# Performance work log

Hardware: AMD Instinct MI355X
Metric: run time of the kernel (lower is better)

The kernel has to match this reference:

```python
import jax, jax.numpy as jnp
import numpy as np

B, N, C, H, KC, STAGES = 8, 4096, 256, 8, 128, 3
C4 = 4 * C
HD = C4 // H
SCALE = (C // H) ** -0.5  # torch uses head_dim of ORIGINAL dim: (256//8)^-0.5


def _l2norm(x, axis):
    # torch: inp / (1e-6 + inp.norm(dim=axis, keepdim=True))
    return x / (1e-6 + jnp.linalg.norm(x, axis=axis, keepdims=True))


def _dta_branch(xc):
    """EM-style clustering on one stream. xc: [B, 4C, N] -> bases [B, 4C, KC]."""
    b, c, n = xc.shape
    # AdaptiveMaxPool1d(KC): N % KC == 0 -> uniform windows of size N//KC
    bases = _l2norm(xc.reshape(b, c, KC, n // KC).max(axis=-1), axis=1)
    xn = xc.transpose(0, 2, 1)  # [B, N, 4C]
    for _ in range(STAGES):
        z = jax.nn.softmax(jnp.einsum('bnc,bck->bnk', xn, bases), axis=2)  # [B,N,KC]
        z = _l2norm(z, axis=1)
        bases = _l2norm(jnp.einsum('bnc,bnk->bck', xn, z), axis=1)  # [B,4C,KC]
    return bases


def setup_inputs() -> dict:
    key = jax.random.key(0)
    ks = jax.random.split(key, 6)
    x = jax.random.normal(ks[0], (B, N, C), jnp.float32)
    Wq = jax.random.normal(ks[1], (C4, C), jnp.float32) * 0.02
    Wk = jax.random.normal(ks[2], (C4, C), jnp.float32) * 0.02
    Wv = jax.random.normal(ks[3], (C4, C), jnp.float32) * 0.02
    Wp = jax.random.normal(ks[4], (C, C4), jnp.float32) * 0.02
    bp = jnp.zeros((C,), jnp.float32)
    return {"x": x, "Wq": Wq, "Wk": Wk, "Wv": Wv, "Wp": Wp, "bp": bp}


def reference(x, Wq, Wk, Wv, Wp, bp):
    # q/k/v projections (bias-free), [B,N,4C]
    q = x @ Wq.T
    k = x @ Wk.T
    v = x @ Wv.T
    # DTA: note torch does `q, k = self.DA(q, k)` where DA(x1,x2) returns
    # (bases_from_x1, bases_from_x2) -> q bases from q-stream, k bases from k-stream.
    qb = _dta_branch(q.transpose(0, 2, 1))  # [B,4C,KC]
    kb = _dta_branch(k.transpose(0, 2, 1))  # [B,4C,KC]
    qh = qb.reshape(B, H, HD, KC)  # == torch q.permute(0,1,3,2): [B,H,hd,KC]
    kh = kb.reshape(B, H, HD, KC)
    vh = v.transpose(0, 2, 1).reshape(B, H, HD, N)  # [B,H,hd,N]
    # att over cluster axis KC -> [B,H,hd,hd]
    att = jax.nn.softmax(jnp.einsum('bhdk,bhek->bhde', qh, kh) * SCALE, axis=-1)
    o = jnp.einsum('bhde,bhen->bhdn', att, vh)  # [B,H,hd,N]
    # rearrange 'b n_h head_dim n -> b n (n_h head_dim)'
    o = o.transpose(0, 3, 1, 2).reshape(B, N, C4)
    return jax.nn.relu(o @ Wp.T + bp)
```

## Files before the change

kernel.cpp:

```cpp
#include <hip/hip_runtime.h>
#include <hip/hip_bf16.h>

#define NSEQ 4096
#define C4   1024
#define SCALE_F 0.17677669529663687f
#define SLC   524288

typedef __attribute__((ext_vector_type(8))) short bf16x8;
typedef __attribute__((ext_vector_type(4))) float f32x4;
typedef __attribute__((ext_vector_type(8))) unsigned short u16x8;
typedef __attribute__((ext_vector_type(4))) unsigned short u16x4;

__device__ __forceinline__ unsigned short f2b(float x){
  union{float f; unsigned u;} v; v.f = x;
  unsigned r = v.u + 0x7fffu + ((v.u>>16)&1u);
  return (unsigned short)(r>>16);
}
__device__ __forceinline__ unsigned mapf(float x){
  unsigned u = __float_as_uint(x);
  return (u & 0x80000000u) ? ~u : (u | 0x80000000u);
}
__device__ __forceinline__ float unmapf(unsigned m){
  unsigned u = (m & 0x80000000u) ? (m ^ 0x80000000u) : ~m;
  return __uint_as_float(u);
}

typedef __attribute__((address_space(1))) void* gas_p;
typedef __attribute__((address_space(3))) void* las_p;
#define GLDS16(gp, lp) __builtin_amdgcn_global_load_lds((gas_p)(gp), (las_p)(lp), 16, 0, 0)

#define WAITVM8() asm volatile("s_waitcnt vmcnt(8)" ::: "memory")
#define WAITVM4() asm volatile("s_waitcnt vmcnt(4)" ::: "memory")
#define WAITVM0() asm volatile("s_waitcnt vmcnt(0)" ::: "memory")
#define WAITLGKM() asm volatile("s_waitcnt lgkmcnt(0)" ::: "memory")
__device__ __forceinline__ void barrier(){
  asm volatile("" ::: "memory");
  __builtin_amdgcn_s_barrier();
  asm volatile("" ::: "memory");
}

__device__ __forceinline__ void stage128x64s(const unsigned short* G, int row0, int ld, int k0,
                                             unsigned short* lds, int tid){
#pragma unroll
  for (int i = 0; i < 4; ++i){
    int cid = i*256 + tid;
    int r = cid >> 3, c8 = cid & 7;
    GLDS16(G + (row0 + r)*ld + k0 + ((c8 ^ (r & 7))*8), lds + cid*8);
  }
}

__device__ __forceinline__ void stage128x128s(const unsigned short* G, int row0, int ld, int k0,
                                              unsigned short* lds, int tid){
#pragma unroll
  for (int i = 0; i < 8; ++i){
    int cid = i*256 + tid;
    int r = cid >> 4, c16 = cid & 15;
    GLDS16(G + (row0 + r)*ld + k0 + ((c16 ^ (r & 7))*8), lds + cid*8);
  }
}

template<int LD, int NK, int MA, int MB>
__device__ __forceinline__ void mma_tiles(const unsigned short* ldsA, const unsigned short* ldsB,
                                          f32x4 acc[4][4], int wr, int wc, int lane){
  const int rowg = lane & 15, q4 = lane >> 4;
#pragma unroll
  for (int kc = 0; kc < NK; ++kc){
    bf16x8 a[4], b[4];
#pragma unroll
    for (int mf = 0; mf < 4; ++mf){
      int row = wr*64 + mf*16 + rowg;
      int off;
      if constexpr (MA == 1) off = ((kc*4 + q4) ^ (row & 7)) * 8;
      else                   off = kc*32 + q4*8;
      a[mf] = *(const bf16x8*)(ldsA + row*LD + off);
    }
#pragma unroll
    for (int nf = 0; nf < 4; ++nf){
      int col = wc*64 + nf*16 + rowg;
      int off;
      if constexpr (MB == 1)      off = ((kc*4 + q4) ^ (col & 7)) * 8;
      else if constexpr (MB == 2) off = (kc*32 + q4*8) ^ ((((col>>3) ^ col) & 7) << 3);
      else                        off = kc*32 + q4*8;
      b[nf] = *(const bf16x8*)(ldsB + col*LD + off);
    }
#pragma unroll
    for (int mf = 0; mf < 4; ++mf)
#pragma unroll
      for (int nf = 0; nf < 4; ++nf)
        acc[mf][nf] = __builtin_amdgcn_mfma_f32_16x16x32_bf16(a[mf], b[nf], acc[mf][nf], 0, 0, 0);
  }
}

__global__ __launch_bounds__(256) void k_cast(const float* __restrict__ src,
                                              unsigned short* __restrict__ dst,
                                              unsigned* __restrict__ pooled, int n){
  int i = (blockIdx.x*256 + threadIdx.x) * 4;
  if (i < n){
    float4 v = *(const float4*)(src + i);
    u16x4 o = { f2b(v.x), f2b(v.y), f2b(v.z), f2b(v.w) };
    *(u16x4*)(dst + i) = o;
  }
  if (blockIdx.x < 2048){
    uint4 z = {0u, 0u, 0u, 0u};
    *(uint4*)(pooled + (blockIdx.x*256 + threadIdx.x)*4) = z;
  }
}

__global__ __launch_bounds__(256) void k_wprep(const float* __restrict__ Wq, const float* __restrict__ Wk,
                                               const float* __restrict__ Wv, const float* __restrict__ Wp,
                                               unsigned short* __restrict__ Wcat,
                                               unsigned short* __restrict__ Wpbf,
                                               unsigned short* __restrict__ WcatT,
                                               unsigned short* __restrict__ WvT){
  int t = blockIdx.x*256 + threadIdx.x;
  int s = blockIdx.y;
  if (s < 3){
    const float* src = (s == 0) ? Wq : (s == 1) ? Wk : Wp;
    unsigned short* dst = (s == 0) ? Wcat : (s == 1) ? (Wcat + 262144) : Wpbf;
    int i = t*4;
    float4 v = *(const float4*)(src + i);
    u16x4 o = { f2b(v.x), f2b(v.y), f2b(v.z), f2b(v.w) };
    *(u16x4*)(dst + i) = o;
  } else {
    const float* src = (s == 3) ? Wv : (s == 4) ? Wq : Wk;
    unsigned short* dst = (s == 3) ? WvT : WcatT;
    int ld  = (s == 3) ? 1024 : 2048;
    int off = (s == 5) ? 1024 : 0;
    int j = t & 255, r0 = (t >> 8) * 4;
    u16x4 o = { f2b(src[(r0+0)*256 + j]), f2b(src[(r0+1)*256 + j]),
                f2b(src[(r0+2)*256 + j]), f2b(src[(r0+3)*256 + j]) };
    *(u16x4*)(dst + j*ld + off + r0) = o;
  }
}

__global__ __launch_bounds__(256) void k_gemm_qk(const unsigned short* __restrict__ xbf,
                                                 const unsigned short* __restrict__ Wcat,
                                                 unsigned* __restrict__ pooled){
  __shared__ __align__(16) unsigned short ldsA[128*64];
  __shared__ __align__(16) unsigned short ldsB[128*64];
  int tid = threadIdx.x, lane = tid & 63, wid = tid >> 6, wr = wid >> 1, wc = wid & 1;
  int m0 = blockIdx.x*128, n0 = blockIdx.y*128;
  f32x4 acc[4][4] = {};
  for (int k0 = 0; k0 < 256; k0 += 64){
    __syncthreads();
    stage128x64s(xbf,  m0, 256, k0, ldsA, tid);
    stage128x64s(Wcat, n0, 256, k0, ldsB, tid);
    __syncthreads();
    mma_tiles<64,2,1,1>(ldsA, ldsB, acc, wr, wc, lane);
  }
  int colg = lane & 15;
  int b = m0 >> 12, kbase = (m0 & 4095) >> 5;
#pragma unroll
  for (int nf = 0; nf < 4; ++nf){
    float wlo = -3e38f, whi = -3e38f;
#pragma unroll
    for (int r = 0; r < 4; ++r){
      wlo = fmaxf(wlo, fmaxf(acc[0][nf][r], acc[1][nf][r]));
      whi = fmaxf(whi, fmaxf(acc[2][nf][r], acc[3][nf][r]));
    }
    wlo = fmaxf(wlo, __shfl_xor(wlo, 16)); wlo = fmaxf(wlo, __shfl_xor(wlo, 32));
    whi = fmaxf(whi, __shfl_xor(whi, 16)); whi = fmaxf(whi, __shfl_xor(whi, 32));
    if (lane < 16){
      int col = n0 + wc*64 + nf*16 + colg;
      int sbp = b + ((col >> 10) << 3);
      int c4 = col & 1023;
      atomicMax(&pooled[(sbp*128 + kbase + wr*2    )*C4 + c4], mapf(wlo));
      atomicMax(&pooled[(sbp*128 + kbase + wr*2 + 1)*C4 + c4], mapf(whi));
    }
  }
}

__global__ __launch_bounds__(256) void k_norm(const float* __restrict__ bRaw,
                                              const unsigned* __restrict__ pooled,
                                              unsigned short* __restrict__ basesT, int S){
  int row = blockIdx.x, tid = threadIdx.x, lane = tid & 63, wid = tid >> 6;
  float4 v;
  if (S == 0){
    uint4 u = *(const uint4*)(pooled + row*C4 + tid*4);
    v.x = unmapf(u.x); v.y = unmapf(u.y); v.z = unmapf(u.z); v.w = unmapf(u.w);
  } else {
    v = *(const float4*)(bRaw + row*C4 + tid*4);
  }
  float ss = v.x*v.x + v.y*v.y + v.z*v.z + v.w*v.w;
  __shared__ float red[5];
#pragma unroll
  for (int o = 32; o; o >>= 1) ss += __shfl_down(ss, o);
  if (lane == 0) red[wid] = ss;
  __syncthreads();
  if (tid == 0) red[4] = 1.f / (1e-6f + sqrtf(red[0] + red[1] + red[2] + red[3]));
  __syncthreads();
  float inv = red[4];
  u16x4 o4 = { f2b(v.x*inv), f2b(v.y*inv), f2b(v.z*inv), f2b(v.w*inv) };
  *(u16x4*)(basesT + row*C4 + tid*4) = o4;
}

__global__ __launch_bounds__(256) void k_pb(const unsigned short* __restrict__ basesT,
                                            const unsigned short* __restrict__ WcatT,
                                            float* __restrict__ part){
  __shared__ __align__(16) unsigned short ldsA[128*64];
  __shared__ __align__(16) unsigned short ldsB[128*64];
  int tid = threadIdx.x, lane = tid & 63, wid = tid >> 6, wr = wid >> 1, wc = wid & 1;
  int n0 = blockIdx.x*128, sb = blockIdx.y, ks = blockIdx.z;
  const unsigned short* A = basesT + sb*(128*C4);
  int off = (sb >= 8) ? 1024 : 0;
  f32x4 acc[4][4] = {};
  for (int t = 0; t < 4; ++t){
    __syncthreads();
    stage128x64s(A,     0,  C4,   ks*256 + t*64, ldsA, tid);
    stage128x64s(WcatT, n0, 2048, off + ks*256 + t*64, ldsB, tid);
    __syncthreads();
    mma_tiles<64,2,1,1>(ldsA, ldsB, acc, wr, wc, lane);
  }
  int colg = lane & 15, rowg = (lane >> 4) * 4;
#pragma unroll
  for (int mf = 0; mf < 4; ++mf)
#pragma unroll
    for (int nf = 0; nf < 4; ++nf)
#pragma unroll
      for (int r = 0; r < 4; ++r)
        part[ks*SLC + (sb*128 + wr*64 + mf*16 + rowg + r)*256 + n0 + wc*64 + nf*16 + colg]
          = acc[mf][nf][r];
}

__global__ __launch_bounds__(256) void k_redgt(const float* __restrict__ src,
                                               unsigned short* __restrict__ dst, int S){
  int i = (blockIdx.x*256 + threadIdx.x) * 4;
  float4 a = {0.f,0.f,0.f,0.f};
  for (int s = 0; s < S; ++s){
    float4 u = *(const float4*)(src + s*SLC + i);
    a.x += u.x; a.y += u.y; a.z += u.z; a.w += u.w;
  }
  u16x4 o = { f2b(a.x), f2b(a.y), f2b(a.z), f2b(a.w) };
  *(u16x4*)(dst + i) = o;
}

__global__ __launch_bounds__(256) void k_gemm_z(const unsigned short* __restrict__ xbf,
                                                const unsigned short* __restrict__ PBT,
                                                unsigned short* __restrict__ zT){
  __shared__ __align__(16) unsigned short smem[32768];
  __shared__ float redb[2][2][128];
  unsigned short* zt = smem;
  int tid = threadIdx.x, lane = tid & 63, wid = tid >> 6, wr = wid >> 1, wc = wid & 1;
  int m0 = blockIdx.x*128, sb = blockIdx.y;
  const unsigned short* A = xbf + (sb & 7)*(NSEQ*256);
  const unsigned short* B = PBT + sb*(128*256);
  f32x4 acc[4][4] = {};
  stage128x64s(A, m0, 256, 0, smem, tid);
  stage128x64s(B, 0,  256, 0, smem + 16384, tid);
  for (int t = 0; t < 4; ++t){
    int cur = t & 1;
    if (t < 3){
      stage128x64s(A, m0, 256, (t+1)*64, smem + (cur^1)*8192, tid);
      stage128x64s(B, 0,  256, (t+1)*64, smem + 16384 + (cur^1)*8192, tid);
      WAITVM8();
    } else WAITVM0();
    barrier();
    mma_tiles<64,2,1,1>(smem + cur*8192, smem + 16384 + cur*8192, acc, wr, wc, lane);
    WAITLGKM();
    barrier();
  }
  int colg = lane & 15, rowg = (lane >> 4) * 4;
  float sm[4][4];
#pragma unroll
  for (int mf = 0; mf < 4; ++mf)
#pragma unroll
    for (int r = 0; r < 4; ++r){
      float m = fmaxf(fmaxf(acc[mf][0][r], acc[mf][1][r]), fmaxf(acc[mf][2][r], acc[mf][3][r]));
#pragma unroll
      for (int o = 1; o < 16; o <<= 1) m = fmaxf(m, __shfl_xor(m, o));
      if (colg == 0) redb[0][wc][wr*64 + mf*16 + rowg + r] = m;
    }
  barrier();
#pragma unroll
  for (int mf = 0; mf < 4; ++mf)
#pragma unroll
    for (int r = 0; r < 4; ++r){
      int idx = wr*64 + mf*16 + rowg + r;
      float m = fmaxf(redb[0][0][idx], redb[0][1][idx]);
      float s = 0.f;
#pragma unroll
      for (int nf = 0; nf < 4; ++nf){
        float e = __expf(acc[mf][nf][r] - m);
        acc[mf][nf][r] = e; s += e;
      }
#pragma unroll
      for (int o = 1; o < 16; o <<= 1) s += __shfl_xor(s, o);
      if (colg == 0) redb[1][wc][idx] = s;
    }
  barrier();
#pragma unroll
  for (int mf = 0; mf < 4; ++mf)
#pragma unroll
    for (int r = 0; r < 4; ++r){
      int idx = wr*64 + mf*16 + rowg + r;
      sm[mf][r] = 1.f / (redb[1][0][idx] + redb[1][1][idx]);
    }
#pragma unroll
  for (int mf = 0; mf < 4; ++mf)
#pragma unroll
    for (int nf = 0; nf < 4; ++nf){
      int k = wc*64 + nf*16 + colg;
      int swz = (k & 7) << 3;
#pragma unroll
      for (int r = 0; r < 4; ++r){
        int n = wr*64 + mf*16 + rowg + r;
        zt[k*128 + (n ^ swz)] = f2b(acc[mf][nf][r] * sm[mf][r]);
      }
    }
  WAITLGKM();
  barrier();
#pragma unroll
  for (int i = 0; i < 8; ++i){
    int cid = i*256 + tid;
    int kk = cid >> 4, j8 = cid & 15;
    int nbase = (j8*8) ^ ((kk & 7) << 3);
    *(uint4*)(zT + sb*(128*NSEQ) + kk*NSEQ + m0 + nbase) = *(const uint4*)(zt + kk*128 + j8*8);
  }
}

__global__ __launch_bounds__(256) void k_gemm_gt(const unsigned short* __restrict__ xbf,
                                                 const unsigned short* __restrict__ zT,
                                                 float* __restrict__ part){
  __shared__ __align__(16) unsigned short ldsA[2][8192];
  __shared__ __align__(16) unsigned short ldsB[2][8192];
  int tid = threadIdx.x, lane = tid & 63, wid = tid >> 6, wr = wid >> 1, wc = wid & 1;
  int c0 = blockIdx.x*128, sb = blockIdx.y, ks = blockIdx.z;
  const unsigned short* xb = xbf + (sb & 7)*(NSEQ*256);
  const unsigned short* Zt = zT + sb*(128*NSEQ);
  int base = ks*512;
  f32x4 acc[4][4] = {};
  u16x8 vB[4];
  int np_[4], c8_[4];
#pragma unroll
  for (int i = 0; i < 4; ++i){
    int cid = i*256 + tid;
    np_[i] = cid >> 4; c8_[i] = cid & 15;
  }
  stage128x64s(Zt, 0, NSEQ, base, ldsA[0], tid);
#pragma unroll
  for (int i = 0; i < 4; ++i)
    vB[i] = *(const u16x8*)(xb + (base + np_[i])*256 + c0 + c8_[i]*8);
  for (int t = 0; t < 8; ++t){
    int cur = t & 1, n0 = base + t*64;
    if (t < 7){
      stage128x64s(Zt, 0, NSEQ, n0 + 64, ldsA[cur^1], tid);
      WAITVM4();
    } else WAITVM0();
#pragma unroll
    for (int i = 0; i < 4; ++i){
#pragma unroll
      for (int j = 0; j < 8; ++j)
        ldsB[cur][(c8_[i]*8 + j)*64 + (np_[i] ^ (((c8_[i] ^ j) & 7) << 3))] = vB[i][j];
    }
    WAITLGKM();
    barrier();
    if (t < 7){
#pragma unroll
      for (int i = 0; i < 4; ++i)
        vB[i] = *(const u16x8*)(xb + (n0 + 64 + np_[i])*256 + c0 + c8_[i]*8);
    }
    mma_tiles<64,2,1,2>(ldsA[cur], ldsB[cur], acc, wr, wc, lane);
    WAITLGKM();
    barrier();
  }
  int colg = lane & 15, rowg = (lane >> 4) * 4;
#pragma unroll
  for (int mf = 0; mf < 4; ++mf)
#pragma unroll
    for (int nf = 0; nf < 4; ++nf)
#pragma unroll
      for (int r = 0; r < 4; ++r)
        part[ks*SLC + (sb*128 + wr*64 + mf*16 + rowg + r)*256 + c0 + wc*64 + nf*16 + colg]
          = acc[mf][nf][r];
}

__global__ __launch_bounds__(256) void k_pbases(const unsigned short* __restrict__ Wcat,
                                                const unsigned short* __restrict__ GTbf,
                                                float* __restrict__ bRaw){
  __shared__ __align__(16) unsigned short ldsA[128*64];
  __shared__ __align__(16) unsigned short ldsB[128*64];
  int tid = threadIdx.x, lane = tid & 63, wid = tid >> 6, wr = wid >> 1, wc = wid & 1;
  int m0 = blockIdx.x*128, sb = blockIdx.y;
  const unsigned short* A = Wcat + ((sb >= 8) ? 1024*256 : 0);
  const unsigned short* B = GTbf + sb*(128*256);
  f32x4 acc[4][4] = {};
  for (int t = 0; t < 4; ++t){
    __syncthreads();
    stage128x64s(A, m0, 256, t*64, ldsA, tid);
    stage128x64s(B, 0,  256, t*64, ldsB, tid);
    __syncthreads();
    mma_tiles<64,2,1,1>(ldsA, ldsB, acc, wr, wc, lane);
  }
  int colg = lane & 15, rowg = (lane >> 4) * 4;
#pragma unroll
  for (int mf = 0; mf < 4; ++mf)
#pragma unroll
    for (int nf = 0; nf < 4; ++nf)
#pragma unroll
      for (int r = 0; r < 4; ++r){
        int c4 = m0 + wr*64 + mf*16 + rowg + r;
        int k  = wc*64 + nf*16 + colg;
        bRaw[(sb*128 + k)*C4 + c4] = acc[mf][nf][r];
      }
}

__global__ __launch_bounds__(256) void k_attnwp(const unsigned short* __restrict__ basesT,
                                                const unsigned short* __restrict__ Wpbf,
                                                unsigned short* __restrict__ WpEff){
  __shared__ __align__(16) char smem[98816];
  unsigned short* Qlt = (unsigned short*)smem;
  unsigned short* Klt = (unsigned short*)(smem + 32768);
  float* scores       = (float*)smem;
  unsigned short* at  = (unsigned short*)(smem + 66048);
  unsigned short* Wl  = (unsigned short*)smem;
  int tid = threadIdx.x, lane = tid & 63, wid = tid >> 6, wr = wid >> 1, wc = wid & 1;
  int m0 = blockIdx.x*128;
  int bh = blockIdx.y, b = bh >> 3, h = bh & 7;
  const unsigned short* Q = basesT + b*(128*C4) + h*128;
  const unsigned short* K = basesT + (8 + b)*(128*C4) + h*128;
#pragma unroll
  for (int i = 0; i < 8; ++i){
    int cid = i*256 + tid, kk = cid >> 4, c8 = cid & 15;
    u16x8 vq = *(const u16x8*)(Q + kk*C4 + c8*8);
    u16x8 vk = *(const u16x8*)(K + kk*C4 + c8*8);
#pragma unroll
    for (int j = 0; j < 8; ++j){
      Qlt[(c8*8 + j)*128 + kk] = vq[j];
      Klt[(c8*8 + j)*128 + kk] = vk[j];
    }
  }
  __syncthreads();
  f32x4 acc[4][4] = {};
  mma_tiles<128,4,0,0>(Qlt, Klt, acc, wr, wc, lane);
  __syncthreads();
  int colg = lane & 15, rowg = (lane >> 4) * 4;
#pragma unroll
  for (int mf = 0; mf < 4; ++mf)
#pragma unroll
    for (int nf = 0; nf < 4; ++nf)
#pragma unroll
      for (int r = 0; r < 4; ++r)
        scores[(wr*64 + mf*16 + rowg + r)*129 + wc*64 + nf*16 + colg] = acc[mf][nf][r] * SCALE_F;
  __syncthreads();
  if (tid < 128){
    float mx = -3e38f;
    for (int j = 0; j < 128; ++j) mx = fmaxf(mx, scores[tid*129 + j]);
    float s = 0.f;
    for (int j = 0; j < 128; ++j){ float e = __expf(scores[tid*129 + j] - mx); scores[tid*129 + j] = e; s += e; }
    float inv = 1.f / s;
    for (int j = 0; j < 128; ++j) at[j*128 + tid] = f2b(scores[tid*129 + j] * inv);
  }
  __syncthreads();
  stage128x128s(Wpbf, m0, C4, h*128, Wl, tid);
  __syncthreads();
  f32x4 acc2[4][4] = {};
  mma_tiles<128,4,1,0>(Wl, at, acc2, wr, wc, lane);
#pragma unroll
  for (int mf = 0; mf < 4; ++mf)
#pragma unroll
    for (int nf = 0; nf < 4; ++nf)
#pragma unroll
      for (int r = 0; r < 4; ++r){
        int row = m0 + wr*64 + mf*16 + rowg + r;
        int col = wc*64 + nf*16 + colg;
        WpEff[b*(256*C4) + row*C4 + h*128 + col] = f2b(acc2[mf][nf][r]);
      }
}

__global__ __launch_bounds__(256) void k_gemm_w2(const unsigned short* __restrict__ WpEff,
                                                 const unsigned short* __restrict__ WvT,
                                                 unsigned short* __restrict__ W2){
  __shared__ __align__(16) unsigned short ldsA[128*64];
  __shared__ __align__(16) unsigned short ldsB[128*64];
  int tid = threadIdx.x, lane = tid & 63, wid = tid >> 6, wr = wid >> 1, wc = wid & 1;
  int m0 = blockIdx.x*128, n0 = blockIdx.y*128, b = blockIdx.z;
  const unsigned short* A = WpEff + b*(256*C4);
  f32x4 acc[4][4] = {};
  for (int k0 = 0; k0 < C4; k0 += 64){
    __syncthreads();
    stage128x64s(A,   m0, C4, k0, ldsA, tid);
    stage128x64s(WvT, n0, C4, k0, ldsB, tid);
    __syncthreads();
    mma_tiles<64,2,1,1>(ldsA, ldsB, acc, wr, wc, lane);
  }
  int colg = lane & 15, rowg = (lane >> 4) * 4;
#pragma unroll
  for (int mf = 0; mf < 4; ++mf)
#pragma unroll
    for (int nf = 0; nf < 4; ++nf)
#pragma unroll
      for (int r = 0; r < 4; ++r){
        int row = m0 + wr*64 + mf*16 + rowg + r;
        int col = n0 + wc*64 + nf*16 + colg;
        W2[b*65536 + row*256 + col] = f2b(acc[mf][nf][r]);
      }
}

__global__ __launch_bounds__(256) void k_gemm_out(const unsigned short* __restrict__ xbf,
                                                  const unsigned short* __restrict__ W2,
                                                  const float* __restrict__ bp,
                                                  float* __restrict__ out){
  __shared__ __align__(16) unsigned short ldsA[2][8192];
  __shared__ __align__(16) unsigned short ldsB[2][8192];
  int tid = threadIdx.x, lane = tid & 63, wid = tid >> 6, wr = wid >> 1, wc = wid & 1;
  int m0 = blockIdx.x*128, n0 = blockIdx.y*128, b = blockIdx.z;
  const unsigned short* A = xbf + b*(NSEQ*256);
  const unsigned short* Bm = W2 + b*65536;
  f32x4 acc[4][4] = {};
  stage128x64s(A,  m0, 256, 0, ldsA[0], tid);
  stage128x64s(Bm, n0, 256, 0, ldsB[0], tid);
  for (int t = 0; t < 4; ++t){
    int cur = t & 1;
    if (t < 3){
      stage128x64s(A,  m0, 256, (t+1)*64, ldsA[cur^1], tid);
      stage128x64s(Bm, n0, 256, (t+1)*64, ldsB[cur^1], tid);
      WAITVM8();
    } else WAITVM0();
    barrier();
    mma_tiles<64,2,1,1>(ldsA[cur], ldsB[cur], acc, wr, wc, lane);
    WAITLGKM();
    barrier();
  }
  int colg = lane & 15, rowg = (lane >> 4) * 4;
#pragma unroll
  for (int mf = 0; mf < 4; ++mf)
#pragma unroll
    for (int nf = 0; nf < 4; ++nf){
      int col = n0 + wc*64 + nf*16 + colg;
      float bias = bp[col];
#pragma unroll
      for (int r = 0; r < 4; ++r){
        int row = m0 + wr*64 + mf*16 + rowg + r;
        out[(b*NSEQ + row)*256 + col] = fmaxf(acc[mf][nf][r] + bias, 0.f);
      }
    }
}

extern "C" void kernel_launch(void* const* d_in, const int* in_sizes, int n_in,
                              void* d_out, int out_size, void* d_ws, size_t ws_size,
                              hipStream_t stream){
  (void)in_sizes; (void)n_in; (void)out_size; (void)ws_size;
  const float* x  = (const float*)d_in[0];
  const float* Wq = (const float*)d_in[1];
  const float* Wk = (const float*)d_in[2];
  const float* Wv = (const float*)d_in[3];
  const float* Wp = (const float*)d_in[4];
  const float* bp = (const float*)d_in[5];
  float* out = (float*)d_out;
  char* ws = (char*)d_ws;

  unsigned short* xbf    = (unsigned short*)(ws + 0);
  unsigned short* zT     = (unsigned short*)(ws + 16777216);
  float*          bPart  = (float*)(ws + 33554432);
  unsigned*       pooled = (unsigned*)(ws + 50331648);
  float*          bRawP  = (float*)(ws + 58720256);
  unsigned short* basesT = (unsigned short*)(ws + 67108864);
  unsigned short* WpEff  = (unsigned short*)(ws + 71303168);
  unsigned short* PBT    = (unsigned short*)(ws + 77594624);
  unsigned short* GTbf   = (unsigned short*)(ws + 78643200);
  unsigned short* Wcat   = (unsigned short*)(ws + 79691776);
  unsigned short* WcatT  = (unsigned short*)(ws + 80740352);
  unsigned short* W2     = (unsigned short*)(ws + 81788928);
  unsigned short* WvT    = (unsigned short*)(ws + 82837504);
  unsigned short* Wpbf   = (unsigned short*)(ws + 83361792);

  k_cast<<<8192, 256, 0, stream>>>(x, xbf, pooled, 8388608);
  k_wprep<<<dim3(256, 6), 256, 0, stream>>>(Wq, Wk, Wv, Wp, Wcat, Wpbf, WcatT, WvT);

  k_gemm_qk<<<dim3(256, 16), 256, 0, stream>>>(xbf, Wcat, pooled);
  k_norm<<<2048, 256, 0, stream>>>(bRawP, pooled, basesT, 0);

  for (int st = 0; st < 3; ++st){
    k_pb<<<dim3(2, 16, 4), 256, 0, stream>>>(basesT, WcatT, bPart);
    k_redgt<<<512, 256, 0, stream>>>(bPart, PBT, 4);
    k_gemm_z<<<dim3(32, 16), 256, 0, stream>>>(xbf, PBT, zT);
    k_gemm_gt<<<dim3(2, 16, 8), 256, 0, stream>>>(xbf, zT, bPart);
    k_redgt<<<512, 256, 0, stream>>>(bPart, GTbf, 8);
    k_pbases<<<dim3(8, 16), 256, 0, stream>>>(Wcat, GTbf, bRawP);
    k_norm<<<2048, 256, 0, stream>>>(bRawP, pooled, basesT, 1);
  }

  k_attnwp<<<dim3(2, 64), 256, 0, stream>>>(basesT, Wpbf, WpEff);
  k_gemm_w2<<<dim3(2, 2, 8), 256, 0, stream>>>(WpEff, WvT, W2);
  k_gemm_out<<<dim3(32, 2, 8), 256, 0, stream>>>(xbf, W2, bp, out);
}
```

Measured before the change: 288.9 us.

## Fuse split-K reductions into GEMM kernels via last-block atomic counter

Removes the separate k_redgt reduction launches by having the last split-K block for each output tile (detected with an atomic counter plus thread fences) sum the partials and write the bf16 result. Counters are reset inside k_norm, which runs before each use. This saves six kernel launches per forward pass and their launch gaps. In exchange the reduction now runs serially in one block per tile, and correctness depends on fence ordering and on the counter reset.

```diff
diff --git a/kernel.cpp b/kernel.cpp
--- a/kernel.cpp
+++ b/kernel.cpp
@@ -172,7 +172,9 @@
 
 __global__ __launch_bounds__(256) void k_norm(const float* __restrict__ bRaw,
                                               const unsigned* __restrict__ pooled,
-                                              unsigned short* __restrict__ basesT, int S){
+                                              unsigned short* __restrict__ basesT,
+                                              unsigned* __restrict__ cnt, int S){
+  if (blockIdx.x == 0 && threadIdx.x < 64) cnt[threadIdx.x] = 0u;
   int row = blockIdx.x, tid = threadIdx.x, lane = tid & 63, wid = tid >> 6;
   float4 v;
   if (S == 0){
@@ -196,9 +198,12 @@
 
 __global__ __launch_bounds__(256) void k_pb(const unsigned short* __restrict__ basesT,
                                             const unsigned short* __restrict__ WcatT,
-                                            float* __restrict__ part){
+                                            float* __restrict__ part,
+                                            unsigned short* __restrict__ PBT,
+                                            unsigned* __restrict__ cnt){
   __shared__ __align__(16) unsigned short ldsA[128*64];
   __shared__ __align__(16) unsigned short ldsB[128*64];
+  __shared__ unsigned lastFlag;
   int tid = threadIdx.x, lane = tid & 63, wid = tid >> 6, wr = wid >> 1, wc = wid & 1;
   int n0 = blockIdx.x*128, sb = blockIdx.y, ks = blockIdx.z;
   const unsigned short* A = basesT + sb*(128*C4);
@@ -220,18 +225,31 @@
       for (int r = 0; r < 4; ++r)
         part[ks*SLC + (sb*128 + wr*64 + mf*16 + rowg + r)*256 + n0 + wc*64 + nf*16 + colg]
           = acc[mf][nf][r];
-}
-
-__global__ __launch_bounds__(256) void k_redgt(const float* __restrict__ src,
-                                               unsigned short* __restrict__ dst, int S){
-  int i = (blockIdx.x*256 + threadIdx.x) * 4;
-  float4 a = {0.f,0.f,0.f,0.f};
-  for (int s = 0; s < S; ++s){
-    float4 u = *(const float4*)(src + s*SLC + i);
-    a.x += u.x; a.y += u.y; a.z += u.z; a.w += u.w;
-  }
-  u16x4 o = { f2b(a.x), f2b(a.y), f2b(a.z), f2b(a.w) };
-  *(u16x4*)(dst + i) = o;
+  WAITVM0();
+  __syncthreads();
+  if (tid == 0){
+    __threadfence();
+    unsigned old = atomicAdd(&cnt[blockIdx.x*16 + sb], 1u);
+    lastFlag = (old == 3u) ? 1u : 0u;
+  }
+  __syncthreads();
+  if (lastFlag){
+    __threadfence();
+    const float* base = part + (sb*128)*256 + n0;
+#pragma unroll
+    for (int i = 0; i < 16; ++i){
+      int e = i*256 + tid;
+      int row = e >> 5, c4 = (e & 31)*4;
+      float4 a = {0.f,0.f,0.f,0.f};
+#pragma unroll
+      for (int s = 0; s < 4; ++s){
+        float4 u = *(const float4*)(base + s*SLC + row*256 + c4);
+        a.x += u.x; a.y += u.y; a.z += u.z; a.w += u.w;
+      }
+      u16x4 o = { f2b(a.x), f2b(a.y), f2b(a.z), f2b(a.w) };
+      *(u16x4*)(PBT + (sb*128 + row)*256 + n0 + c4) = o;
+    }
+  }
 }
 
 __global__ __launch_bounds__(256) void k_gemm_z(const unsigned short* __restrict__ xbf,
@@ -320,9 +338,12 @@
 
 __global__ __launch_bounds__(256) void k_gemm_gt(const unsigned short* __restrict__ xbf,
                                                  const unsigned short* __restrict__ zT,
-                                                 float* __restrict__ part){
+                                                 float* __restrict__ part,
+                                                 unsigned short* __restrict__ GTbf,
+                                                 unsigned* __restrict__ cnt){
   __shared__ __align__(16) unsigned short ldsA[2][8192];
   __shared__ __align__(16) unsigned short ldsB[2][8192];
+  __shared__ unsigned lastFlag;
   int tid = threadIdx.x, lane = tid & 63, wid = tid >> 6, wr = wid >> 1, wc = wid & 1;
   int c0 = blockIdx.x*128, sb = blockIdx.y, ks = blockIdx.z;
   const unsigned short* xb = xbf + (sb & 7)*(NSEQ*256);
@@ -372,6 +393,31 @@
       for (int r = 0; r < 4; ++r)
         part[ks*SLC + (sb*128 + wr*64 + mf*16 + rowg + r)*256 + c0 + wc*64 + nf*16 + colg]
           = acc[mf][nf][r];
+  WAITVM0();
+  __syncthreads();
+  if (tid == 0){
+    __threadfence();
+    unsigned old = atomicAdd(&cnt[32 + blockIdx.x*16 + sb], 1u);
+    lastFlag = (old == 7u) ? 1u : 0u;
+  }
+  __syncthreads();
+  if (lastFlag){
+    __threadfence();
+    const float* basep = part + (sb*128)*256 + c0;
+#pragma unroll
+    for (int i = 0; i < 16; ++i){
+      int e = i*256 + tid;
+      int row = e >> 5, c4 = (e & 31)*4;
+      float4 a = {0.f,0.f,0.f,0.f};
+#pragma unroll
+      for (int s = 0; s < 8; ++s){
+        float4 u = *(const float4*)(basep + s*SLC + row*256 + c4);
+        a.x += u.x; a.y += u.y; a.z += u.z; a.w += u.w;
+      }
+      u16x4 o = { f2b(a.x), f2b(a.y), f2b(a.z), f2b(a.w) };
+      *(u16x4*)(GTbf + (sb*128 + row)*256 + c0 + c4) = o;
+    }
+  }
 }
 
 __global__ __launch_bounds__(256) void k_pbases(const unsigned short* __restrict__ Wcat,
@@ -563,21 +609,20 @@
   unsigned short* W2     = (unsigned short*)(ws + 81788928);
   unsigned short* WvT    = (unsigned short*)(ws + 82837504);
   unsigned short* Wpbf   = (unsigned short*)(ws + 83361792);
+  unsigned*       cnt    = (unsigned*)(ws + 83886080);
 
   k_cast<<<8192, 256, 0, stream>>>(x, xbf, pooled, 8388608);
   k_wprep<<<dim3(256, 6), 256, 0, stream>>>(Wq, Wk, Wv, Wp, Wcat, Wpbf, WcatT, WvT);
 
   k_gemm_qk<<<dim3(256, 16), 256, 0, stream>>>(xbf, Wcat, pooled);
-  k_norm<<<2048, 256, 0, stream>>>(bRawP, pooled, basesT, 0);
+  k_norm<<<2048, 256, 0, stream>>>(bRawP, pooled, basesT, cnt, 0);
 
   for (int st = 0; st < 3; ++st){
-    k_pb<<<dim3(2, 16, 4), 256, 0, stream>>>(basesT, WcatT, bPart);
-    k_redgt<<<512, 256, 0, stream>>>(bPart, PBT, 4);
+    k_pb<<<dim3(2, 16, 4), 256, 0, stream>>>(basesT, WcatT, bPart, PBT, cnt);
     k_gemm_z<<<dim3(32, 16), 256, 0, stream>>>(xbf, PBT, zT);
-    k_gemm_gt<<<dim3(2, 16, 8), 256, 0, stream>>>(xbf, zT, bPart);
-    k_redgt<<<512, 256, 0, stream>>>(bPart, GTbf, 8);
+    k_gemm_gt<<<dim3(2, 16, 8), 256, 0, stream>>>(xbf, zT, bPart, GTbf, cnt);
     k_pbases<<<dim3(8, 16), 256, 0, stream>>>(Wcat, GTbf, bRawP);
-    k_norm<<<2048, 256, 0, stream>>>(bRawP, pooled, basesT, 1);
+    k_norm<<<2048, 256, 0, stream>>>(bRawP, pooled, basesT, cnt, 1);
   }
 
   k_attnwp<<<dim3(2, 64), 256, 0, stream>>>(basesT, Wpbf, WpEff);
```

Measured after the change: 345.2 us. 1.2x slower.

## Fold bases projection through precomputed weight Gram matrix in EM iterations

Applied to the files above, without the earlier changes.

Precomputes the 256x256 Gram matrix of the Q and K weights once, then in EM stages 2 and 3 computes the normalized projected bases directly from the reduced G^T via a small fused GEMM with the Gram matrix. The norm uses the quadratic form g^T Gram g. This replaces the per-stage k_pbases, k_norm, k_pb and reduction launches with one 16-block kernel. It adds a bf16 Gram matrix and a norm computed from it, which may change rounding, and the fused kernel runs on only 16 blocks.

```diff
diff --git a/kernel.cpp b/kernel.cpp
--- a/kernel.cpp
+++ b/kernel.cpp
@@ -11,6 +11,9 @@
 typedef __attribute__((ext_vector_type(8))) unsigned short u16x8;
 typedef __attribute__((ext_vector_type(4))) unsigned short u16x4;
 
+__device__ __forceinline__ float b2f(unsigned short b){
+  union{unsigned u; float f;} v; v.u = ((unsigned)b)<<16; return v.f;
+}
 __device__ __forceinline__ unsigned short f2b(float x){
   union{float f; unsigned u;} v; v.f = x;
   unsigned r = v.u + 0x7fffu + ((v.u>>16)&1u);
@@ -57,6 +60,11 @@
     int r = cid >> 4, c16 = cid & 15;
     GLDS16(G + (row0 + r)*ld + k0 + ((c16 ^ (r & 7))*8), lds + cid*8);
   }
+}
+
+__device__ __forceinline__ float gtread(const unsigned short* gtile, int row, int c){
+  int p = c >> 6, cc = c & 63, c8g = cc >> 3, j = cc & 7;
+  return b2f(gtile[p*8192 + row*64 + ((c8g ^ (row & 7)) << 3) + j]);
 }
 
 template<int LD, int NK, int MA, int MB>
@@ -133,6 +141,31 @@
   }
 }
 
+__global__ __launch_bounds__(256) void k_gram(const unsigned short* __restrict__ WcatT,
+                                              unsigned short* __restrict__ Gram){
+  __shared__ __align__(16) unsigned short ldsA[128*64];
+  __shared__ __align__(16) unsigned short ldsB[128*64];
+  int tid = threadIdx.x, lane = tid & 63, wid = tid >> 6, wr = wid >> 1, wc = wid & 1;
+  int m0 = blockIdx.x*128, n0 = blockIdx.y*128, off = blockIdx.z*1024;
+  f32x4 acc[4][4] = {};
+  for (int k0 = 0; k0 < 1024; k0 += 64){
+    __syncthreads();
+    stage128x64s(WcatT, m0, 2048, off + k0, ldsA, tid);
+    stage128x64s(WcatT, n0, 2048, off + k0, ldsB, tid);
+    __syncthreads();
+    mma_tiles<64,2,1,1>(ldsA, ldsB, acc, wr, wc, lane);
+  }
+  int colg = lane & 15, rowg = (lane >> 4) * 4;
+#pragma unroll
+  for (int mf = 0; mf < 4; ++mf)
+#pragma unroll
+    for (int nf = 0; nf < 4; ++nf)
+#pragma unroll
+      for (int r = 0; r < 4; ++r)
+        Gram[blockIdx.z*65536 + (m0 + wr*64 + mf*16 + rowg + r)*256 + n0 + wc*64 + nf*16 + colg]
+          = f2b(acc[mf][nf][r]);
+}
+
 __global__ __launch_bounds__(256) void k_gemm_qk(const unsigned short* __restrict__ xbf,
                                                  const unsigned short* __restrict__ Wcat,
                                                  unsigned* __restrict__ pooled){
@@ -232,6 +265,66 @@
   }
   u16x4 o = { f2b(a.x), f2b(a.y), f2b(a.z), f2b(a.w) };
   *(u16x4*)(dst + i) = o;
+}
+
+__global__ __launch_bounds__(256) void k_normpb(const unsigned short* __restrict__ GTbf,
+                                                const unsigned short* __restrict__ Gram,
+                                                unsigned short* __restrict__ PBT){
+  __shared__ __align__(16) unsigned short gtile[128*256];
+  __shared__ __align__(16) unsigned short btile[128*64];
+  __shared__ float redn[2][128];
+  int tid = threadIdx.x, lane = tid & 63, wid = tid >> 6, wr = wid >> 1, wc = wid & 1;
+  int sb = blockIdx.x;
+  const unsigned short* GTsb = GTbf + sb*(128*256);
+  const unsigned short* Gm = Gram + ((sb >= 8) ? 65536 : 0);
+#pragma unroll
+  for (int p = 0; p < 4; ++p)
+    stage128x64s(GTsb, 0, 256, p*64, gtile + p*8192, tid);
+  f32x4 accA[4][4] = {}, accB[4][4] = {};
+  for (int t = 0; t < 4; ++t){
+    __syncthreads();
+    stage128x64s(Gm, 0, 256, t*64, btile, tid);
+    __syncthreads();
+    mma_tiles<64,2,1,1>(gtile + t*8192, btile, accA, wr, wc, lane);
+  }
+  for (int t = 0; t < 4; ++t){
+    __syncthreads();
+    stage128x64s(Gm, 128, 256, t*64, btile, tid);
+    __syncthreads();
+    mma_tiles<64,2,1,1>(gtile + t*8192, btile, accB, wr, wc, lane);
+  }
+  int colg = lane & 15, rowg = (lane >> 4) * 4;
+#pragma unroll
+  for (int mf = 0; mf < 4; ++mf)
+#pragma unroll
+    for (int r = 0; r < 4; ++r){
+      int row = wr*64 + mf*16 + rowg + r;
+      float d = 0.f;
+#pragma unroll
+      for (int nf = 0; nf < 4; ++nf){
+        int cA = wc*64 + nf*16 + colg;
+        d += accA[mf][nf][r] * gtread(gtile, row, cA);
+        d += accB[mf][nf][r] * gtread(gtile, row, 128 + cA);
+      }
+#pragma unroll
+      for (int o = 1; o < 16; o <<= 1) d += __shfl_xor(d, o);
+      if (colg == 0) redn[wc][row] = d;
+    }
+  __syncthreads();
+#pragma unroll
+  for (int mf = 0; mf < 4; ++mf)
+#pragma unroll
+    for (int r = 0; r < 4; ++r){
+      int row = wr*64 + mf*16 + rowg + r;
+      float nrm2 = fmaxf(redn[0][row] + redn[1][row], 0.f);
+      float inv = 1.f / (1e-6f + sqrtf(nrm2));
+#pragma unroll
+      for (int nf = 0; nf < 4; ++nf){
+        int cA = wc*64 + nf*16 + colg;
+        PBT[(sb*128 + row)*256 + cA]       = f2b(accA[mf][nf][r] * inv);
+        PBT[(sb*128 + row)*256 + 128 + cA] = f2b(accB[mf][nf][r] * inv);
+      }
+    }
 }
 
 __global__ __launch_bounds__(256) void k_gemm_z(const unsigned short* __restrict__ xbf,
@@ -563,22 +656,30 @@
   unsigned short* W2     = (unsigned short*)(ws + 81788928);
   unsigned short* WvT    = (unsigned short*)(ws + 82837504);
   unsigned short* Wpbf   = (unsigned short*)(ws + 83361792);
+  unsigned short* Gram   = (unsigned short*)(ws + 83886080);
 
   k_cast<<<8192, 256, 0, stream>>>(x, xbf, pooled, 8388608);
   k_wprep<<<dim3(256, 6), 256, 0, stream>>>(Wq, Wk, Wv, Wp, Wcat, Wpbf, WcatT, WvT);
+  k_gram<<<dim3(2, 2, 2), 256, 0, stream>>>(WcatT, Gram);
 
   k_gemm_qk<<<dim3(256, 16), 256, 0, stream>>>(xbf, Wcat, pooled);
   k_norm<<<2048, 256, 0, stream>>>(bRawP, pooled, basesT, 0);
 
-  for (int st = 0; st < 3; ++st){
-    k_pb<<<dim3(2, 16, 4), 256, 0, stream>>>(basesT, WcatT, bPart);
-    k_redgt<<<512, 256, 0, stream>>>(bPart, PBT, 4);
+  k_pb<<<dim3(2, 16, 4), 256, 0, stream>>>(basesT, WcatT, bPart);
+  k_redgt<<<512, 256, 0, stream>>>(bPart, PBT, 4);
+  k_gemm_z<<<dim3(32, 16), 256, 0, stream>>>(xbf, PBT, zT);
+  k_gemm_gt<<<dim3(2, 16, 8), 256, 0, stream>>>(xbf, zT, bPart);
+  k_redgt<<<512, 256, 0, stream>>>(bPart, GTbf, 8);
+
+  for (int st = 1; st < 3; ++st){
+    k_normpb<<<16, 256, 0, stream>>>(GTbf, Gram, PBT);
     k_gemm_z<<<dim3(32, 16), 256, 0, stream>>>(xbf, PBT, zT);
     k_gemm_gt<<<dim3(2, 16, 8), 256, 0, stream>>>(xbf, zT, bPart);
     k_redgt<<<512, 256, 0, stream>>>(bPart, GTbf, 8);
-    k_pbases<<<dim3(8, 16), 256, 0, stream>>>(Wcat, GTbf, bRawP);
-    k_norm<<<2048, 256, 0, stream>>>(bRawP, pooled, basesT, 1);
-  }
+  }
+
+  k_pbases<<<dim3(8, 16), 256, 0, stream>>>(Wcat, GTbf, bRawP);
+  k_norm<<<2048, 256, 0, stream>>>(bRawP, pooled, basesT, 1);
 
   k_attnwp<<<dim3(2, 64), 256, 0, stream>>>(basesT, Wpbf, WpEff);
   k_gemm_w2<<<dim3(2, 2, 8), 256, 0, stream>>>(WpEff, WvT, W2);
```

New measurement: 293.0 us. No clear change (+1.4%).
